# Optimization experiments

Hardware: AMD Instinct MI355X
Metric: run time of the kernel (lower is better)

## Reference

```python
import jax, jax.numpy as jnp
import numpy as np

IMAGE_W = IMAGE_H = 608
TOP_N = 1000
MIN_SCORE = 0.05
NMS_THR = 0.5
MAX_DET = 100
B = 8
NUM_CLASSES = 80
STRIDES = [32, 16, 8]
ANCHOR_WH = {32: [[116, 90], [156, 198], [373, 326]],
             16: [[30, 61], [62, 45], [59, 119]],
             8: [[10, 13], [16, 30], [33, 23]]}


def _make_anchors(stride):
    # anchors layout [B,g,g,3,5] = (grid_x, grid_y, anchor_w*stride, anchor_h*stride, stride)
    g = IMAGE_W // stride
    ys, xs = jnp.meshgrid(jnp.arange(g, dtype=jnp.float32),
                          jnp.arange(g, dtype=jnp.float32), indexing='ij')
    grid = jnp.broadcast_to(jnp.stack([xs, ys], -1)[:, :, None, :], (g, g, 3, 2))
    wh = jnp.asarray(ANCHOR_WH[stride], dtype=jnp.float32) * stride
    wh = jnp.broadcast_to(wh[None, None, :, :], (g, g, 3, 2))
    s = jnp.full((g, g, 3, 1), float(stride), dtype=jnp.float32)
    a = jnp.concatenate([grid, wh, s], -1)
    return jnp.broadcast_to(a[None], (B, g, g, 3, 5))


def setup_inputs() -> dict:
    key = jax.random.key(0)
    ks = jax.random.split(key, 9)
    inp = {}
    for i, stride in enumerate(STRIDES):
        g = IMAGE_W // stride
        inp[f'obj{i}'] = jax.random.normal(ks[3 * i + 0], (B, g, g, 3, 1), jnp.float32)
        inp[f'reg{i}'] = jax.random.normal(ks[3 * i + 1], (B, g, g, 3, 4), jnp.float32)
        inp[f'cls{i}'] = jax.random.normal(ks[3 * i + 2], (B, g, g, 3, NUM_CLASSES), jnp.float32)
        inp[f'anchors{i}'] = _make_anchors(stride)
    return inp


def _decode_level(obj, reg, cls, anch):
    Bn = obj.shape[0]
    obj = jax.nn.sigmoid(obj.reshape(Bn, -1))                       # [B,N]
    cls = jax.nn.sigmoid(cls.reshape(Bn, -1, cls.shape[-1]))        # [B,N,C]
    reg = reg.reshape(Bn, -1, 4)
    anch = anch.reshape(Bn, -1, 5)
    ctr = (jax.nn.sigmoid(reg[..., 0:2]) + anch[..., 0:2]) * anch[..., 4:5]
    wh = jnp.exp(reg[..., 2:4]) * anch[..., 2:4] / anch[..., 4:5]
    x1y1 = ctr - 0.5 * wh
    x2y2 = wh + x1y1
    boxes = jnp.concatenate([x1y1, x2y2], -1).astype(jnp.int32)     # trunc toward zero == torch .int()
    boxes = jnp.stack([jnp.maximum(boxes[..., 0], 0),
                       jnp.maximum(boxes[..., 1], 0),
                       jnp.minimum(boxes[..., 2], IMAGE_W - 1),
                       jnp.minimum(boxes[..., 3], IMAGE_H - 1)], -1)
    scores = jnp.max(cls, axis=-1) * obj
    classes = jnp.argmax(cls, axis=-1).astype(jnp.int32)
    if scores.shape[1] >= TOP_N:
        scores, idx = jax.lax.top_k(scores, TOP_N)
        classes = jnp.take_along_axis(classes, idx, axis=1)
        boxes = jnp.take_along_axis(boxes, idx[..., None], axis=1)
    return scores, classes, boxes


def _nms_one_image(scores, classes, boxes):
    # scores [N], classes int32 [N], boxes int32 [N,4]
    N = scores.shape[0]
    valid = scores > MIN_SCORE
    s = jnp.where(valid, scores, -1.0)
    order = jnp.argsort(-s)
    s = s[order]
    valid = valid[order]
    cls_f = classes[order].astype(jnp.float32)
    b = boxes[order].astype(jnp.float32)
    areas = (b[:, 2] - b[:, 0]) * (b[:, 3] - b[:, 1])
    idxs = jnp.arange(N)

    def body(i, keep):
        box = b[i]
        xx1 = jnp.maximum(box[0], b[:, 0])
        yy1 = jnp.maximum(box[1], b[:, 1])
        xx2 = jnp.minimum(box[2], b[:, 2])
        yy2 = jnp.minimum(box[3], b[:, 3])
        inter = jnp.maximum(xx2 - xx1, 0.0) * jnp.maximum(yy2 - yy1, 0.0)
        iou = inter / (areas[i] + areas - inter)
        suppress = keep[i] & (idxs > i) & (iou > NMS_THR)
        return keep & ~suppress

    keep = jax.lax.fori_loop(0, N, body, valid)
    pos = jnp.cumsum(keep) - 1                       # output slot of each kept box
    slot = jnp.where(keep & (pos < MAX_DET), pos, MAX_DET)  # overflow/dropped -> dump slot
    out_s = jnp.full((MAX_DET + 1,), -1.0, jnp.float32).at[slot].set(s)[:MAX_DET]
    out_c = jnp.full((MAX_DET + 1,), -1.0, jnp.float32).at[slot].set(cls_f)[:MAX_DET]
    out_b = jnp.full((MAX_DET + 1, 4), -1.0, jnp.float32).at[slot].set(b)[:MAX_DET]
    return out_s, out_c, out_b


def _forward(obj0, obj1, obj2, reg0, reg1, reg2, cls0, cls1, cls2,
             anchors0, anchors1, anchors2):
    objs = [obj0, obj1, obj2]
    regs = [reg0, reg1, reg2]
    clss = [cls0, cls1, cls2]
    anchs = [anchors0, anchors1, anchors2]
    sc, cl, bx = [], [], []
    for o, r, c, a in zip(objs, regs, clss, anchs):
        s_, c_, b_ = _decode_level(o, r, c, a)
        sc.append(s_); cl.append(c_); bx.append(b_)
    scores = jnp.concatenate(sc, axis=1)
    classes = jnp.concatenate(cl, axis=1)
    boxes = jnp.concatenate(bx, axis=1)
    return jax.vmap(_nms_one_image)(scores, classes, boxes)


def reference(obj0, obj1, obj2, reg0, reg1, reg2, cls0, cls1, cls2,
              anchors0, anchors1, anchors2):
    return _forward(obj0, obj1, obj2, reg0, reg1, reg2, cls0, cls1, cls2,
                    anchors0, anchors1, anchors2)
```

## Files before the change

kernel.cpp:

```cpp
#include <hip/hip_runtime.h>
#include <math.h>

constexpr int BATCH   = 8;
constexpr int NUM_CLS = 80;
constexpr int N0 = 19 * 19 * 3;
constexpr int N1 = 38 * 38 * 3;
constexpr int N2 = 76 * 76 * 3;
constexpr int OFF1 = N0;
constexpr int OFF2 = N0 + N1;
constexpr int NTOT = N0 + N1 + N2;
constexpr int TOPN = 1000;
constexpr int NSEL = 3 * TOPN;
constexpr int MAXDET = 100;
constexpr float MIN_SCORE_F = 0.05f;
constexpr int IMG_MAX = 607;

__device__ __forceinline__ float sigmoidf_(float x) {
    return 1.0f / (1.0f + expf(-x));
}

__constant__ float AWH[3][3][2] = {
    {{116.f, 90.f}, {156.f, 198.f}, {373.f, 326.f}},
    {{ 30.f, 61.f}, { 62.f,  45.f}, { 59.f, 119.f}},
    {{ 10.f, 13.f}, { 16.f,  30.f}, { 33.f,  23.f}},
};

__device__ __forceinline__ bool iou_gt(float4 a, float4 c) {
    float ai = (a.z - a.x) * (a.w - a.y);
    float aj = (c.z - c.x) * (c.w - c.y);
    float xx1 = fmaxf(a.x, c.x);
    float yy1 = fmaxf(a.y, c.y);
    float xx2 = fminf(a.z, c.z);
    float yy2 = fminf(a.w, c.w);
    float inter = fmaxf(xx2 - xx1, 0.0f) * fmaxf(yy2 - yy1, 0.0f);
    float uni = ai + aj - inter;
    return (inter > 0.5f * uni) && (inter > 0.0f);
}

__global__ __launch_bounds__(256) void k_decode(
    const float* __restrict__ obj0, const float* __restrict__ reg0,
    const float* __restrict__ cls0,
    const float* __restrict__ obj1, const float* __restrict__ reg1,
    const float* __restrict__ cls1,
    const float* __restrict__ obj2, const float* __restrict__ reg2,
    const float* __restrict__ cls2,
    unsigned long long* __restrict__ decKey, float* __restrict__ decC,
    float* __restrict__ decB, int* __restrict__ gflagImg, int* __restrict__ fbCursor)
{
    if (blockIdx.x == 0 && threadIdx.x < 32) {
        if (threadIdx.x < 8)  gflagImg[threadIdx.x] = 0;
        if (threadIdx.x < 24) fbCursor[threadIdx.x] = 0;
    }

    __shared__ float sBest[64];
    __shared__ int   sCls[64];

    int g0 = blockIdx.x * 64;
    int t  = threadIdx.x;

    {
        int q  = t >> 2;
        int lq = t & 3;
        int idx = g0 + q;
        if (idx < BATCH * NTOT) {
            int b  = idx / NTOT;
            int na = idx - b * NTOT;
            const float* cls; int Nl, n;
            if (na < OFF1)      { cls = cls0; Nl = N0; n = na; }
            else if (na < OFF2) { cls = cls1; Nl = N1; n = na - OFF1; }
            else                { cls = cls2; Nl = N2; n = na - OFF2; }
            size_t bn = (size_t)b * Nl + n;

            const float4* cv = reinterpret_cast<const float4*>(cls + bn * NUM_CLS);
            float best = -1.0f; int bc = 0;
            #pragma unroll
            for (int k = 0; k < 5; ++k) {
                int m = lq + 4 * k;
                float4 v = cv[m];
                float s;
                s = sigmoidf_(v.x); if (s > best) { best = s; bc = 4 * m + 0; }
                s = sigmoidf_(v.y); if (s > best) { best = s; bc = 4 * m + 1; }
                s = sigmoidf_(v.z); if (s > best) { best = s; bc = 4 * m + 2; }
                s = sigmoidf_(v.w); if (s > best) { best = s; bc = 4 * m + 3; }
            }
            #pragma unroll
            for (int d = 1; d <= 2; d <<= 1) {
                float ob = __shfl_xor(best, d);
                int   oc = __shfl_xor(bc, d);
                if (ob > best || (ob == best && oc < bc)) { best = ob; bc = oc; }
            }
            if (lq == 0) { sBest[q] = best; sCls[q] = bc; }
        }
    }
    __syncthreads();

    if (t < 64) {
        int idx = g0 + t;
        if (idx < BATCH * NTOT) {
            int b  = idx / NTOT;
            int na = idx - b * NTOT;
            const float *obj, *reg;
            int Nl, n, lvl, g;
            float st;
            if (na < OFF1)      { obj = obj0; reg = reg0; Nl = N0; n = na;        lvl = 0; g = 19; st = 32.f; }
            else if (na < OFF2) { obj = obj1; reg = reg1; Nl = N1; n = na - OFF1; lvl = 1; g = 38; st = 16.f; }
            else                { obj = obj2; reg = reg2; Nl = N2; n = na - OFF2; lvl = 2; g = 76; st = 8.f;  }
            size_t bn = (size_t)b * Nl + n;

            float so    = sigmoidf_(obj[bn]);
            float score = sBest[t] * so;
            int   bc    = sCls[t];

            int a    = n % 3;
            int cell = n / 3;
            int gx   = cell % g;
            int gy   = cell / g;
            float ax = (float)gx, ay = (float)gy;
            float aw = AWH[lvl][a][0], ah = AWH[lvl][a][1];

            float4 rv = reinterpret_cast<const float4*>(reg)[bn];
            float cx = (sigmoidf_(rv.x) + ax) * st;
            float cy = (sigmoidf_(rv.y) + ay) * st;
            float w  = expf(rv.z) * aw;
            float h  = expf(rv.w) * ah;
            float x1f = cx - 0.5f * w;
            float y1f = cy - 0.5f * h;
            float x2f = w + x1f;
            float y2f = h + y1f;
            int x1 = (int)x1f, y1 = (int)y1f, x2 = (int)x2f, y2 = (int)y2f;
            x1 = (x1 < 0) ? 0 : x1;
            y1 = (y1 < 0) ? 0 : y1;
            x2 = (x2 > IMG_MAX) ? IMG_MAX : x2;
            y2 = (y2 > IMG_MAX) ? IMG_MAX : y2;

            size_t gg = (size_t)b * NTOT + na;
            decKey[gg] = ((unsigned long long)__float_as_uint(score) << 15) | (unsigned)(Nl - n);
            decC[gg] = (float)bc;
            reinterpret_cast<float4*>(decB)[gg] =
                make_float4((float)x1, (float)y1, (float)x2, (float)y2);
        }
    }
}

constexpr int NBIN  = 4096;
constexpr int STCAP = 2048;

__global__ __launch_bounds__(1024) void k_select(
    const unsigned long long* __restrict__ decKey, const float* __restrict__ decC,
    const float* __restrict__ decB, float* __restrict__ selS, float* __restrict__ selC,
    float* __restrict__ selB, unsigned long long* __restrict__ selKey,
    int* __restrict__ gflagImg, int* __restrict__ fbCursor)
{
    __shared__ unsigned hist[NBIN];
    __shared__ unsigned cum[NBIN];
    __shared__ unsigned wscan[32];
    __shared__ unsigned long long stKey[STCAP];
    __shared__ int stIdx[STCAP];
    __shared__ int sTot; __shared__ int sOvf;
    __shared__ int sBstar; __shared__ int sNeed;

    int b   = blockIdx.x / 3;
    int lvl = blockIdx.x % 3;
    int off = (lvl == 0) ? 0 : (lvl == 1) ? OFF1 : OFF2;
    int Nl  = (lvl == 0) ? N0 : (lvl == 1) ? N1 : N2;
    int tid = threadIdx.x;
    int lane = tid & 63;
    int wv   = tid >> 6;

    const unsigned long long* keys = decKey + (size_t)b * NTOT + off;

    for (int t = tid; t < NBIN; t += 1024) hist[t] = 0;
    if (tid == 0) { sTot = 0; sOvf = 0; }
    __syncthreads();

    for (int t = tid; t < Nl; t += 1024)
        atomicAdd(&hist[(unsigned)(keys[t] >> 33)], 1u);
    __syncthreads();

    {
        uint4 hh = reinterpret_cast<uint4*>(hist)[tid];
        reinterpret_cast<uint4*>(hist)[tid] = make_uint4(0u, 0u, 0u, 0u);
        unsigned ssum = hh.x + hh.y + hh.z + hh.w;

        unsigned sfx = ssum;
        #pragma unroll
        for (int d = 1; d < 64; d <<= 1) {
            unsigned o = __shfl_down(sfx, d);
            if (lane + d < 64) sfx += o;
        }
        if (lane == 0) wscan[wv] = sfx;
        __syncthreads();
        if (tid < 16) {
            unsigned v = wscan[tid];
            unsigned s2 = v;
            #pragma unroll
            for (int d = 1; d < 16; d <<= 1) {
                unsigned o = __shfl_down(s2, d);
                if (tid + d < 16) s2 += o;
            }
            wscan[16 + tid] = s2 - v;
        }
        __syncthreads();
        unsigned Tt = wscan[16 + wv] + (sfx - ssum);
        unsigned c3 = Tt;
        unsigned c2 = c3 + hh.w;
        unsigned c1 = c2 + hh.z;
        unsigned c0 = c1 + hh.y;
        reinterpret_cast<uint4*>(cum)[tid] = make_uint4(c0, c1, c2, c3);
    }
    __syncthreads();

    for (int t = tid; t < Nl; t += 1024) {
        unsigned long long k = keys[t];
        unsigned bin = (unsigned)(k >> 33);
        if (cum[bin] < (unsigned)TOPN) {
            unsigned c = atomicAdd(&hist[bin], 1u);
            unsigned p = cum[bin] + c;
            if (p < STCAP) { stKey[p] = k; stIdx[p] = t; }
            else sOvf = 1;
        }
    }
    __syncthreads();

    {
        uint4 hh = reinterpret_cast<uint4*>(hist)[tid];
        uint4 cc = reinterpret_cast<uint4*>(cum)[tid];
        unsigned loc = 0;
        if (cc.x < (unsigned)TOPN) loc += hh.x;
        if (cc.y < (unsigned)TOPN) loc += hh.y;
        if (cc.z < (unsigned)TOPN) loc += hh.z;
        if (cc.w < (unsigned)TOPN) loc += hh.w;
        #pragma unroll
        for (int d = 1; d < 64; d <<= 1) loc += __shfl_down(loc, d);
        if (lane == 0 && loc) atomicAdd(&sTot, (int)loc);
    }
    __syncthreads();

    auto writeOut = [&](int t, int r) {
        size_t g = (size_t)b * NTOT + off + t;
        unsigned long long k = keys[t];
        float sraw = __uint_as_float((unsigned)(k >> 15));
        float strn = (sraw > MIN_SCORE_F) ? sraw : -1.0f;
        int G = off + t;
        unsigned long long gk =
            ((unsigned long long)(__float_as_uint(sraw) | 0x80000000u) << 16) |
            (unsigned)(NTOT - G);
        int o = b * NSEL + lvl * TOPN + r;
        selS[o] = strn;
        selC[o] = decC[g];
        selKey[o] = gk;
        reinterpret_cast<float4*>(selB)[o] = reinterpret_cast<const float4*>(decB)[g];
    };

    if (sOvf == 0) {
        int M = sTot;
        for (int p = tid; p < M; p += 1024) {
            unsigned long long k = stKey[p];
            unsigned bin = (unsigned)(k >> 33);
            unsigned start = cum[bin], end = start + hist[bin];
            int r = (int)start;
            for (unsigned q = start; q < end; ++q) r += (stKey[q] > k) ? 1 : 0;
            if (r < TOPN) writeOut(stIdx[p], r);
        }
    } else {
        if (tid == 0) {
            gflagImg[b] = 1;
            int B = 0;
            for (int bin = NBIN - 1; bin >= 0; --bin) {
                if (cum[bin] <= (unsigned)(TOPN - 1) &&
                    cum[bin] + hist[bin] > (unsigned)(TOPN - 1)) { B = bin; break; }
            }
            sBstar = B; sNeed = TOPN - (int)cum[B];
        }
        __syncthreads();
        int Bstar = sBstar, need = sNeed;
        for (int t = tid; t < Nl; t += 1024) {
            unsigned long long k = keys[t];
            int bin = (int)(unsigned)(k >> 33);
            bool em = false;
            if (bin > Bstar) em = true;
            else if (bin == Bstar) {
                int r = 0;
                for (int j = 0; j < Nl; ++j) {
                    unsigned long long kj = keys[j];
                    r += ((int)(unsigned)(kj >> 33) == Bstar && kj > k) ? 1 : 0;
                }
                em = (r < need);
            }
            if (em) {
                int r = atomicAdd(&fbCursor[b * 3 + lvl], 1);
                writeOut(t, r);
            }
        }
    }
}

__global__ __launch_bounds__(1024) void k_nms(
    const float* __restrict__ selS, const float* __restrict__ selC,
    const float* __restrict__ selB, const unsigned long long* __restrict__ selKey,
    const int* __restrict__ gflagImg,
    float* __restrict__ out)
{
    __shared__ union {
        unsigned long long keys[NSEL];
        float4 boxes[NSEL];
    } U;
    __shared__ int ord[NSEL];
    __shared__ float4 keptBox[MAXDET];
    __shared__ int keptRank[MAXDET];
    __shared__ int sPos; __shared__ int sNValid;

    int b = blockIdx.x, tid = threadIdx.x;
    const float* S = selS + b * NSEL;

    for (int t = tid; t < NSEL; t += 1024) U.keys[t] = selKey[b * NSEL + t];
    if (tid == 0) sNValid = 0;
    __syncthreads();
    int fb = gflagImg[b];

    int myT[3], myR[3];
    int nMine = 0;
    int nvLoc = 0;
    for (int t = tid; t < NSEL; t += 1024) {
        unsigned long long k = U.keys[t];
        int rank;
        if (!fb) {
            int l = t / TOPN;
            rank = t - l * TOPN;
            #pragma unroll
            for (int m = 0; m < 3; ++m) {
                if (m == l) continue;
                int base = m * TOPN, lo = 0, hi = TOPN;
                while (lo < hi) {
                    int mid = (lo + hi) >> 1;
                    if (U.keys[base + mid] > k) lo = mid + 1; else hi = mid;
                }
                rank += lo;
            }
        } else {
            int r = 0;
            for (int j = 0; j < NSEL; ++j) r += (U.keys[j] > k) ? 1 : 0;
            rank = r;
        }
        myT[nMine] = t; myR[nMine] = rank; nMine++;
        if (S[t] > MIN_SCORE_F) nvLoc++;
    }
    #pragma unroll
    for (int d = 1; d < 64; d <<= 1) nvLoc += __shfl_down(nvLoc, d);
    if ((tid & 63) == 0 && nvLoc) atomicAdd(&sNValid, nvLoc);
    __syncthreads();

    for (int q = 0; q < nMine; ++q) {
        float4 bb = reinterpret_cast<const float4*>(selB)[b * NSEL + myT[q]];
        U.boxes[myR[q]] = bb;
        ord[myR[q]] = myT[q];
    }
    __syncthreads();

    if (tid < 64) {
        int lane = tid;
        int nValid = sNValid;
        int pos = 0;
        int nW = (nValid + 63) >> 6;
        for (int w = 0; w < nW && pos < MAXDET; ++w) {
            int j = w * 64 + lane;
            float4 bx = (j < NSEL) ? U.boxes[j]
                                   : make_float4(4e8f, 4e8f, -4e8f, -4e8f);
            bool valid = (j < nValid);
            bool sup = false;
            for (int q = 0; q < pos; ++q)
                sup = sup || iou_gt(keptBox[q], bx);
            unsigned long long live = __ballot(valid && !sup);
            while (live) {
                int p = __ffsll(live) - 1;
                if (lane == 0) keptRank[pos] = w * 64 + p;
                if (lane == p) keptBox[pos] = bx;
                pos++;
                if (pos >= MAXDET) break;
                float kx = __shfl(bx.x, p), ky = __shfl(bx.y, p);
                float kz = __shfl(bx.z, p), kw = __shfl(bx.w, p);
                bool hit = iou_gt(make_float4(kx, ky, kz, kw), bx);
                live &= ~__ballot(hit);
                live &= ~(1ull << p);
            }
        }
        if (lane == 0) sPos = pos;
    }
    __syncthreads();

    int pos = sPos;
    const float* C = selC + b * NSEL;
    float* out_s = out + b * MAXDET;
    float* out_c = out + BATCH * MAXDET + b * MAXDET;
    float* out_b = out + 2 * BATCH * MAXDET + (size_t)b * MAXDET * 4;
    for (int t = tid; t < MAXDET; t += 1024) {
        if (t < pos) {
            int i = keptRank[t];
            int o = ord[i];
            float4 bb = U.boxes[i];
            out_s[t] = S[o];
            out_c[t] = C[o];
            out_b[t * 4 + 0] = bb.x; out_b[t * 4 + 1] = bb.y;
            out_b[t * 4 + 2] = bb.z; out_b[t * 4 + 3] = bb.w;
        } else {
            out_s[t] = -1.0f; out_c[t] = -1.0f;
            out_b[t * 4 + 0] = -1.0f; out_b[t * 4 + 1] = -1.0f;
            out_b[t * 4 + 2] = -1.0f; out_b[t * 4 + 3] = -1.0f;
        }
    }
}

extern "C" void kernel_launch(void* const* d_in, const int* in_sizes, int n_in,
                              void* d_out, int out_size, void* d_ws, size_t ws_size,
                              hipStream_t stream) {
    (void)n_in; (void)out_size; (void)ws_size;

    bool dict = (in_sizes[2] == BATCH * N0 * NUM_CLS);
    const float *obj[3], *reg[3], *cls[3];
    for (int l = 0; l < 3; ++l) {
        obj[l] = (const float*)d_in[dict ? 4 * l + 0 : l];
        reg[l] = (const float*)d_in[dict ? 4 * l + 1 : 3 + l];
        cls[l] = (const float*)d_in[dict ? 4 * l + 2 : 6 + l];
    }

    char* ws = (char*)d_ws;
    size_t off = 0;
    auto take = [&](size_t bytes) -> void* {
        void* p = ws + off;
        off += (bytes + 255) & ~(size_t)255;
        return p;
    };
    int*                 gflagImg = (int*)take(BATCH * sizeof(int));
    int*                 fbCursor = (int*)take(BATCH * 3 * sizeof(int));
    unsigned long long*  decKey   = (unsigned long long*)take((size_t)BATCH * NTOT * 8);
    float*               decC     = (float*)take((size_t)BATCH * NTOT * 4);
    float*               decB     = (float*)take((size_t)BATCH * NTOT * 16);
    float*               selS     = (float*)take((size_t)BATCH * NSEL * 4);
    float*               selC     = (float*)take((size_t)BATCH * NSEL * 4);
    float*               selB     = (float*)take((size_t)BATCH * NSEL * 16);
    unsigned long long*  selKey   = (unsigned long long*)take((size_t)BATCH * NSEL * 8);

    int totalDec = BATCH * NTOT;
    k_decode<<<(totalDec + 63) / 64, 256, 0, stream>>>(
        obj[0], reg[0], cls[0],
        obj[1], reg[1], cls[1],
        obj[2], reg[2], cls[2],
        decKey, decC, decB, gflagImg, fbCursor);

    k_select<<<BATCH * 3, 1024, 0, stream>>>(decKey, decC, decB,
                                             selS, selC, selB, selKey,
                                             gflagImg, fbCursor);

    k_nms<<<BATCH, 1024, 0, stream>>>(selS, selC, selB, selKey, gflagImg,
                                      (float*)d_out);
}
```

Measured before the change: 172.1 us.

## Fuse top-k select and NMS kernels via per-image completion counter

Merges the per-level selection kernel and the per-image NMS kernel into one launch. Each level block increments a per-image counter after a threadfence, and the level-0 block spin-waits until all three levels finish before running NMS, reusing the selection LDS through a union. This removes one kernel launch and its inter-kernel gap. The cost is a spin-wait that relies on all 24 blocks being co-resident, plus idle time for the level-0 block while it waits.

```diff
diff --git a/kernel.cpp b/kernel.cpp
--- a/kernel.cpp
+++ b/kernel.cpp
@@ -45,10 +45,12 @@
     const float* __restrict__ obj2, const float* __restrict__ reg2,
     const float* __restrict__ cls2,
     unsigned long long* __restrict__ decKey, float* __restrict__ decC,
-    float* __restrict__ decB, int* __restrict__ gflagImg, int* __restrict__ fbCursor)
+    float* __restrict__ decB, int* __restrict__ gflagImg, int* __restrict__ fbCursor,
+    int* __restrict__ lvlDone)
 {
     if (blockIdx.x == 0 && threadIdx.x < 32) {
         if (threadIdx.x < 8)  gflagImg[threadIdx.x] = 0;
+        if (threadIdx.x < 8)  lvlDone[threadIdx.x] = 0;
         if (threadIdx.x < 24) fbCursor[threadIdx.x] = 0;
     }
 
@@ -145,19 +147,31 @@
 constexpr int NBIN  = 4096;
 constexpr int STCAP = 2048;
 
-__global__ __launch_bounds__(1024) void k_select(
+__global__ __launch_bounds__(1024) void k_select_nms(
     const unsigned long long* __restrict__ decKey, const float* __restrict__ decC,
     const float* __restrict__ decB, float* __restrict__ selS, float* __restrict__ selC,
     float* __restrict__ selB, unsigned long long* __restrict__ selKey,
-    int* __restrict__ gflagImg, int* __restrict__ fbCursor)
+    int* __restrict__ gflagImg, int* __restrict__ fbCursor,
+    int* __restrict__ lvlDone, float* __restrict__ out)
 {
-    __shared__ unsigned hist[NBIN];
-    __shared__ unsigned cum[NBIN];
-    __shared__ unsigned wscan[32];
-    __shared__ unsigned long long stKey[STCAP];
-    __shared__ int stIdx[STCAP];
+    __shared__ union LdsU {
+        struct {
+            unsigned hist[NBIN];
+            unsigned cum[NBIN];
+            unsigned wscan[32];
+            unsigned long long stKey[STCAP];
+            int stIdx[STCAP];
+        } sel;
+        struct {
+            union { unsigned long long keys[NSEL]; float4 boxes[NSEL]; } U;
+            int ord[NSEL];
+        } nms;
+    } L;
+    __shared__ float4 keptBox[MAXDET];
+    __shared__ int keptRank[MAXDET];
     __shared__ int sTot; __shared__ int sOvf;
     __shared__ int sBstar; __shared__ int sNeed;
+    __shared__ int sPos; __shared__ int sNValid;
 
     int b   = blockIdx.x / 3;
     int lvl = blockIdx.x % 3;
@@ -167,150 +181,155 @@
     int lane = tid & 63;
     int wv   = tid >> 6;
 
-    const unsigned long long* keys = decKey + (size_t)b * NTOT + off;
-
-    for (int t = tid; t < NBIN; t += 1024) hist[t] = 0;
-    if (tid == 0) { sTot = 0; sOvf = 0; }
-    __syncthreads();
-
-    for (int t = tid; t < Nl; t += 1024)
-        atomicAdd(&hist[(unsigned)(keys[t] >> 33)], 1u);
-    __syncthreads();
-
     {
-        uint4 hh = reinterpret_cast<uint4*>(hist)[tid];
-        reinterpret_cast<uint4*>(hist)[tid] = make_uint4(0u, 0u, 0u, 0u);
-        unsigned ssum = hh.x + hh.y + hh.z + hh.w;
-
-        unsigned sfx = ssum;
-        #pragma unroll
-        for (int d = 1; d < 64; d <<= 1) {
-            unsigned o = __shfl_down(sfx, d);
-            if (lane + d < 64) sfx += o;
-        }
-        if (lane == 0) wscan[wv] = sfx;
+        unsigned* hist = L.sel.hist;
+        unsigned* cum  = L.sel.cum;
+        unsigned* wscan = L.sel.wscan;
+        unsigned long long* stKey = L.sel.stKey;
+        int* stIdx = L.sel.stIdx;
+
+        const unsigned long long* keys = decKey + (size_t)b * NTOT + off;
+
+        for (int t = tid; t < NBIN; t += 1024) hist[t] = 0;
+        if (tid == 0) { sTot = 0; sOvf = 0; }
         __syncthreads();
-        if (tid < 16) {
-            unsigned v = wscan[tid];
-            unsigned s2 = v;
+
+        for (int t = tid; t < Nl; t += 1024)
+            atomicAdd(&hist[(unsigned)(keys[t] >> 33)], 1u);
+        __syncthreads();
+
+        {
+            uint4 hh = reinterpret_cast<uint4*>(hist)[tid];
+            reinterpret_cast<uint4*>(hist)[tid] = make_uint4(0u, 0u, 0u, 0u);
+            unsigned ssum = hh.x + hh.y + hh.z + hh.w;
+
+            unsigned sfx = ssum;
             #pragma unroll
-            for (int d = 1; d < 16; d <<= 1) {
-                unsigned o = __shfl_down(s2, d);
-                if (tid + d < 16) s2 += o;
-            }
-            wscan[16 + tid] = s2 - v;
+            for (int d = 1; d < 64; d <<= 1) {
+                unsigned o = __shfl_down(sfx, d);
+                if (lane + d < 64) sfx += o;
+            }
+            if (lane == 0) wscan[wv] = sfx;
+            __syncthreads();
+            if (tid < 16) {
+                unsigned v = wscan[tid];
+                unsigned s2 = v;
+                #pragma unroll
+                for (int d = 1; d < 16; d <<= 1) {
+                    unsigned o = __shfl_down(s2, d);
+                    if (tid + d < 16) s2 += o;
+                }
+                wscan[16 + tid] = s2 - v;
+            }
+            __syncthreads();
+            unsigned Tt = wscan[16 + wv] + (sfx - ssum);
+            unsigned c3 = Tt;
+            unsigned c2 = c3 + hh.w;
+            unsigned c1 = c2 + hh.z;
+            unsigned c0 = c1 + hh.y;
+            reinterpret_cast<uint4*>(cum)[tid] = make_uint4(c0, c1, c2, c3);
         }
         __syncthreads();
-        unsigned Tt = wscan[16 + wv] + (sfx - ssum);
-        unsigned c3 = Tt;
-        unsigned c2 = c3 + hh.w;
-        unsigned c1 = c2 + hh.z;
-        unsigned c0 = c1 + hh.y;
-        reinterpret_cast<uint4*>(cum)[tid] = make_uint4(c0, c1, c2, c3);
-    }
-    __syncthreads();
-
-    for (int t = tid; t < Nl; t += 1024) {
-        unsigned long long k = keys[t];
-        unsigned bin = (unsigned)(k >> 33);
-        if (cum[bin] < (unsigned)TOPN) {
-            unsigned c = atomicAdd(&hist[bin], 1u);
-            unsigned p = cum[bin] + c;
-            if (p < STCAP) { stKey[p] = k; stIdx[p] = t; }
-            else sOvf = 1;
-        }
-    }
-    __syncthreads();
-
-    {
-        uint4 hh = reinterpret_cast<uint4*>(hist)[tid];
-        uint4 cc = reinterpret_cast<uint4*>(cum)[tid];
-        unsigned loc = 0;
-        if (cc.x < (unsigned)TOPN) loc += hh.x;
-        if (cc.y < (unsigned)TOPN) loc += hh.y;
-        if (cc.z < (unsigned)TOPN) loc += hh.z;
-        if (cc.w < (unsigned)TOPN) loc += hh.w;
-        #pragma unroll
-        for (int d = 1; d < 64; d <<= 1) loc += __shfl_down(loc, d);
-        if (lane == 0 && loc) atomicAdd(&sTot, (int)loc);
-    }
-    __syncthreads();
-
-    auto writeOut = [&](int t, int r) {
-        size_t g = (size_t)b * NTOT + off + t;
-        unsigned long long k = keys[t];
-        float sraw = __uint_as_float((unsigned)(k >> 15));
-        float strn = (sraw > MIN_SCORE_F) ? sraw : -1.0f;
-        int G = off + t;
-        unsigned long long gk =
-            ((unsigned long long)(__float_as_uint(sraw) | 0x80000000u) << 16) |
-            (unsigned)(NTOT - G);
-        int o = b * NSEL + lvl * TOPN + r;
-        selS[o] = strn;
-        selC[o] = decC[g];
-        selKey[o] = gk;
-        reinterpret_cast<float4*>(selB)[o] = reinterpret_cast<const float4*>(decB)[g];
-    };
-
-    if (sOvf == 0) {
-        int M = sTot;
-        for (int p = tid; p < M; p += 1024) {
-            unsigned long long k = stKey[p];
-            unsigned bin = (unsigned)(k >> 33);
-            unsigned start = cum[bin], end = start + hist[bin];
-            int r = (int)start;
-            for (unsigned q = start; q < end; ++q) r += (stKey[q] > k) ? 1 : 0;
-            if (r < TOPN) writeOut(stIdx[p], r);
-        }
-    } else {
-        if (tid == 0) {
-            gflagImg[b] = 1;
-            int B = 0;
-            for (int bin = NBIN - 1; bin >= 0; --bin) {
-                if (cum[bin] <= (unsigned)(TOPN - 1) &&
-                    cum[bin] + hist[bin] > (unsigned)(TOPN - 1)) { B = bin; break; }
-            }
-            sBstar = B; sNeed = TOPN - (int)cum[B];
-        }
-        __syncthreads();
-        int Bstar = sBstar, need = sNeed;
+
         for (int t = tid; t < Nl; t += 1024) {
             unsigned long long k = keys[t];
-            int bin = (int)(unsigned)(k >> 33);
-            bool em = false;
-            if (bin > Bstar) em = true;
-            else if (bin == Bstar) {
-                int r = 0;
-                for (int j = 0; j < Nl; ++j) {
-                    unsigned long long kj = keys[j];
-                    r += ((int)(unsigned)(kj >> 33) == Bstar && kj > k) ? 1 : 0;
+            unsigned bin = (unsigned)(k >> 33);
+            if (cum[bin] < (unsigned)TOPN) {
+                unsigned c = atomicAdd(&hist[bin], 1u);
+                unsigned p = cum[bin] + c;
+                if (p < STCAP) { stKey[p] = k; stIdx[p] = t; }
+                else sOvf = 1;
+            }
+        }
+        __syncthreads();
+
+        {
+            uint4 hh = reinterpret_cast<uint4*>(hist)[tid];
+            uint4 cc = reinterpret_cast<uint4*>(cum)[tid];
+            unsigned loc = 0;
+            if (cc.x < (unsigned)TOPN) loc += hh.x;
+            if (cc.y < (unsigned)TOPN) loc += hh.y;
+            if (cc.z < (unsigned)TOPN) loc += hh.z;
+            if (cc.w < (unsigned)TOPN) loc += hh.w;
+            #pragma unroll
+            for (int d = 1; d < 64; d <<= 1) loc += __shfl_down(loc, d);
+            if (lane == 0 && loc) atomicAdd(&sTot, (int)loc);
+        }
+        __syncthreads();
+
+        auto writeOut = [&](int t, int r) {
+            size_t g = (size_t)b * NTOT + off + t;
+            unsigned long long k = keys[t];
+            float sraw = __uint_as_float((unsigned)(k >> 15));
+            float strn = (sraw > MIN_SCORE_F) ? sraw : -1.0f;
+            int G = off + t;
+            unsigned long long gk =
+                ((unsigned long long)(__float_as_uint(sraw) | 0x80000000u) << 16) |
+                (unsigned)(NTOT - G);
+            int o = b * NSEL + lvl * TOPN + r;
+            selS[o] = strn;
+            selC[o] = decC[g];
+            selKey[o] = gk;
+            reinterpret_cast<float4*>(selB)[o] = reinterpret_cast<const float4*>(decB)[g];
+        };
+
+        if (sOvf == 0) {
+            int M = sTot;
+            for (int p = tid; p < M; p += 1024) {
+                unsigned long long k = stKey[p];
+                unsigned bin = (unsigned)(k >> 33);
+                unsigned start = cum[bin], end = start + hist[bin];
+                int r = (int)start;
+                for (unsigned q = start; q < end; ++q) r += (stKey[q] > k) ? 1 : 0;
+                if (r < TOPN) writeOut(stIdx[p], r);
+            }
+        } else {
+            if (tid == 0) {
+                gflagImg[b] = 1;
+                int B = 0;
+                for (int bin = NBIN - 1; bin >= 0; --bin) {
+                    if (cum[bin] <= (unsigned)(TOPN - 1) &&
+                        cum[bin] + hist[bin] > (unsigned)(TOPN - 1)) { B = bin; break; }
                 }
-                em = (r < need);
-            }
-            if (em) {
-                int r = atomicAdd(&fbCursor[b * 3 + lvl], 1);
-                writeOut(t, r);
-            }
-        }
-    }
-}
-
-__global__ __launch_bounds__(1024) void k_nms(
-    const float* __restrict__ selS, const float* __restrict__ selC,
-    const float* __restrict__ selB, const unsigned long long* __restrict__ selKey,
-    const int* __restrict__ gflagImg,
-    float* __restrict__ out)
-{
-    __shared__ union {
-        unsigned long long keys[NSEL];
-        float4 boxes[NSEL];
-    } U;
-    __shared__ int ord[NSEL];
-    __shared__ float4 keptBox[MAXDET];
-    __shared__ int keptRank[MAXDET];
-    __shared__ int sPos; __shared__ int sNValid;
-
-    int b = blockIdx.x, tid = threadIdx.x;
+                sBstar = B; sNeed = TOPN - (int)cum[B];
+            }
+            __syncthreads();
+            int Bstar = sBstar, need = sNeed;
+            for (int t = tid; t < Nl; t += 1024) {
+                unsigned long long k = keys[t];
+                int bin = (int)(unsigned)(k >> 33);
+                bool em = false;
+                if (bin > Bstar) em = true;
+                else if (bin == Bstar) {
+                    int r = 0;
+                    for (int j = 0; j < Nl; ++j) {
+                        unsigned long long kj = keys[j];
+                        r += ((int)(unsigned)(kj >> 33) == Bstar && kj > k) ? 1 : 0;
+                    }
+                    em = (r < need);
+                }
+                if (em) {
+                    int r = atomicAdd(&fbCursor[b * 3 + lvl], 1);
+                    writeOut(t, r);
+                }
+            }
+        }
+    }
+
+    __threadfence();
+    __syncthreads();
+    if (tid == 0) atomicAdd(&lvlDone[b], 1);
+
+    if (lvl != 0) return;
+
+    if (tid == 0) {
+        while (atomicAdd(&lvlDone[b], 0) < 3) __builtin_amdgcn_s_sleep(8);
+    }
+    __syncthreads();
+    __threadfence();
+
+    auto& U = L.nms.U;
+    int* ord = L.nms.ord;
     const float* S = selS + b * NSEL;
 
     for (int t = tid; t < NSEL; t += 1024) U.keys[t] = selKey[b * NSEL + t];
@@ -358,7 +377,6 @@
     __syncthreads();
 
     if (tid < 64) {
-        int lane = tid;
         int nValid = sNValid;
         int pos = 0;
         int nW = (nValid + 63) >> 6;
@@ -432,6 +450,7 @@
     };
     int*                 gflagImg = (int*)take(BATCH * sizeof(int));
     int*                 fbCursor = (int*)take(BATCH * 3 * sizeof(int));
+    int*                 lvlDone  = (int*)take(BATCH * sizeof(int));
     unsigned long long*  decKey   = (unsigned long long*)take((size_t)BATCH * NTOT * 8);
     float*               decC     = (float*)take((size_t)BATCH * NTOT * 4);
     float*               decB     = (float*)take((size_t)BATCH * NTOT * 16);
@@ -445,12 +464,10 @@
         obj[0], reg[0], cls[0],
         obj[1], reg[1], cls[1],
         obj[2], reg[2], cls[2],
-        decKey, decC, decB, gflagImg, fbCursor);
-
-    k_select<<<BATCH * 3, 1024, 0, stream>>>(decKey, decC, decB,
-                                             selS, selC, selB, selKey,
-                                             gflagImg, fbCursor);
-
-    k_nms<<<BATCH, 1024, 0, stream>>>(selS, selC, selB, selKey, gflagImg,
-                                      (float*)d_out);
+        decKey, decC, decB, gflagImg, fbCursor, lvlDone);
+
+    k_select_nms<<<BATCH * 3, 1024, 0, stream>>>(decKey, decC, decB,
+                                                 selS, selC, selB, selKey,
+                                                 gflagImg, fbCursor, lvlDone,
+                                                 (float*)d_out);
 }
```

Result: slower. 182.1 us (+5.9%).
